# Performance work log

Measured on AMD Instinct MI355X. Metric: run time of the kernel, lower is better.

Reference implementation:

```python
import jax, jax.numpy as jnp
import numpy as np

DIM = 96
HEADS = 3
HEAD_DIM = 32
MLP_DIM = 384
WS = 4  # window size (cubic)


def _rel_indices(ws):
    # relative position indices for a ws^3 window, offset to [0, 2*ws-2]
    coords = np.stack(np.meshgrid(np.arange(ws), np.arange(ws), np.arange(ws), indexing='ij'), -1).reshape(-1, 3)
    rel = coords[:, None, :] - coords[None, :, :] + (ws - 1)  # (n, n, 3)
    return jnp.asarray(rel, dtype=jnp.int32)


def _layer_norm(x, g, b, eps=1e-5):
    m = x.mean(-1, keepdims=True)
    v = x.var(-1, keepdims=True)
    return (x - m) * jax.lax.rsqrt(v + eps) * g + b


def setup_inputs() -> dict:
    key = jax.random.key(0)
    ks = jax.random.split(key, 12)
    inner = HEADS * HEAD_DIM
    s = lambda fan_in: 1.0 / np.sqrt(fan_in)
    return {
        'x': jax.random.normal(ks[0], (2, 128, 128, 8, DIM), dtype=jnp.float32),
        'ln1_g': jnp.ones((DIM,), jnp.float32),
        'ln1_b': jnp.zeros((DIM,), jnp.float32),
        'w_qkv': jax.random.normal(ks[1], (DIM, 3 * inner), jnp.float32) * s(DIM),
        'w_out': jax.random.normal(ks[2], (inner, DIM), jnp.float32) * s(inner),
        'b_out': jnp.zeros((DIM,), jnp.float32),
        'pos_tab': jax.random.normal(ks[3], (2 * WS - 1, 2 * WS - 1, 2 * WS - 1), jnp.float32),
        'ln2_g': jnp.ones((DIM,), jnp.float32),
        'ln2_b': jnp.zeros((DIM,), jnp.float32),
        'w1': jax.random.normal(ks[4], (DIM, MLP_DIM), jnp.float32) * s(DIM),
        'b1': jnp.zeros((MLP_DIM,), jnp.float32),
        'w2': jax.random.normal(ks[5], (MLP_DIM, DIM), jnp.float32) * s(MLP_DIM),
        'b2': jnp.zeros((DIM,), jnp.float32),
    }


def reference(x, ln1_g, ln1_b, w_qkv, w_out, b_out, pos_tab, ln2_g, ln2_b, w1, b1, w2, b2):
    B, H, W, D, C = x.shape
    h, d, ws = HEADS, HEAD_DIM, WS
    nH, nW, nD = H // ws, W // ws, D // ws
    n = ws ** 3
    scale = d ** -0.5

    # --- window attention block (PreNorm + Residual) ---
    y = _layer_norm(x, ln1_g, ln1_b)
    qkv = y @ w_qkv  # (B,H,W,D,3*h*d)
    qkv = qkv.reshape(B, nH, ws, nW, ws, nD, ws, 3, h, d)
    qkv = qkv.transpose(7, 0, 8, 1, 3, 5, 2, 4, 6, 9)  # (3,B,h,nH,nW,nD,ws,ws,ws,d)
    qkv = qkv.reshape(3, B, h, nH * nW * nD, n, d)
    q, k, v = qkv[0], qkv[1], qkv[2]

    attn = jnp.einsum('bhwid,bhwjd->bhwij', q, k) * scale  # (B,h,nw,n,n)
    rel = _rel_indices(ws)
    bias = pos_tab[rel[..., 0], rel[..., 1], rel[..., 2]]  # (n,n)
    attn = jax.nn.softmax(attn + bias, axis=-1)
    o = jnp.einsum('bhwij,bhwjd->bhwid', attn, v)  # (B,h,nw,n,d)

    o = o.reshape(B, h, nH, nW, nD, ws, ws, ws, d)
    o = o.transpose(0, 2, 5, 3, 6, 4, 7, 1, 8).reshape(B, H, W, D, h * d)
    x = x + (o @ w_out + b_out)

    # --- MLP block (PreNorm + Residual), GELU exact to match nn.GELU ---
    y = _layer_norm(x, ln2_g, ln2_b)
    y = jax.nn.gelu(y @ w1 + b1, approximate=False) @ w2 + b2
    return x + y
```

## Files before the change

### kernel.cpp

```cpp
#include <hip/hip_runtime.h>

#define DIM 96
#define HEADS 3
#define HD 32
#define MLPD 384
#define NTOK 64
#define YP 104
#define KP 104
#define QKP 200
#define VP 72
#define WSP 104
#define HP 40
#define W1P 104
#define W2P 40
#define W2SP 32
#define X1P 100
#define CH 32
#define NCH 12
#define WQT_OFF 147456
#define WOT_OFF 175104
#define WS2_NEEDED 368640

typedef unsigned short ushort_t;
typedef unsigned int uint_t;
typedef __attribute__((ext_vector_type(8))) short bf16x8;
typedef __attribute__((ext_vector_type(4))) float f32x4;

__device__ inline float b2f(ushort_t u) {
    return __uint_as_float(((uint_t)u) << 16);
}
__device__ inline ushort_t f2b(float f) {
    uint_t u = __float_as_uint(f);
    uint_t r = u + 0x7FFFu + ((u >> 16) & 1u);
    return (ushort_t)(r >> 16);
}
__device__ inline void split2(float v, ushort_t& hi, ushort_t& lo) {
    hi = f2b(v);
    float d = v - b2f(hi);
    lo = f2b(d);
}
__device__ inline void split_pack2(float v0, float v1, uint_t& hi2, uint_t& lo2) {
    uint_t u0 = __float_as_uint(v0), u1 = __float_as_uint(v1);
    hi2 = __builtin_amdgcn_perm(u1, u0, 0x07060302u);
    float d0 = v0 - __uint_as_float(u0 & 0xFFFF0000u);
    float d1 = v1 - __uint_as_float(u1 & 0xFFFF0000u);
    lo2 = __builtin_amdgcn_perm(__float_as_uint(d1), __float_as_uint(d0), 0x07060302u);
}
__device__ inline size_t grow(int bb, int wh, int ww, int wd, int t) {
    return ((size_t)((bb * 128 + wh * 4 + (t >> 4)) * 128 + ww * 4 + ((t >> 2) & 3)) * 8
            + wd * 4 + (t & 3));
}
__device__ inline float gelu_fast(float v) {
    float z = v * 0.70710678118654752f;
    float az = fabsf(z);
    float k = __frcp_rn(1.0f + 0.3275911f * az);
    float poly = k * (0.254829592f + k * (-0.284496736f + k * (1.421413741f
                 + k * (-1.453152027f + k * 1.061405429f))));
    float e = 1.0f - poly * __expf(-az * az);
    float erfv = copysignf(e, z);
    return 0.5f * v * (1.0f + erfv);
}

__global__ __launch_bounds__(256) void prep_weights(
    const float* __restrict__ w1, const float* __restrict__ w2,
    const float* __restrict__ w_qkv, const float* __restrict__ w_out,
    ushort_t* __restrict__ wt)
{
    int idx = blockIdx.x * 256 + threadIdx.x;
    if (idx >= 96 * MLPD) return;
    {
        int k = idx / MLPD, col = idx % MLPD;
        ushort_t h, l;
        split2(w1[idx], h, l);
        wt[col * 96 + k] = h;
        wt[36864 + col * 96 + k] = l;
    }
    {
        int k = idx / 96, n = idx % 96;
        int c = k >> 5, f = k & 31;
        int p = ((f & 15) >> 2) * 8 + (f >> 4) * 4 + (f & 3);
        ushort_t h, l;
        split2(w2[idx], h, l);
        wt[73728  + n * MLPD + c * 32 + p] = h;
        wt[110592 + n * MLPD + c * 32 + p] = l;
    }
    if (idx < 288 * 96) {
        int f = idx / 96, k = idx % 96;
        wt[WQT_OFF + f * 96 + k] = f2b(w_qkv[k * 288 + f]);
    }
    if (idx < 96 * 96) {
        int n = idx / 96, k = idx % 96;
        wt[WOT_OFF + n * 96 + k] = f2b(w_out[k * 96 + n]);
    }
}

__global__ __launch_bounds__(256, 4) void swin_fused_kernel(
    const float* __restrict__ x,
    const float* __restrict__ ln1_g, const float* __restrict__ ln1_b,
    const ushort_t* __restrict__ wt,
    const float* __restrict__ b_out, const float* __restrict__ pos_tab,
    const float* __restrict__ ln2_g, const float* __restrict__ ln2_b,
    const float* __restrict__ b1v, const float* __restrict__ b2v,
    float* __restrict__ out)
{
    __shared__ __align__(16) ushort_t smem[20224];
    ushort_t* ybuf = smem;
    ushort_t* kbuf = smem + 6656;
    ushort_t* vbuf = smem + 13312;
    float* x1f = reinterpret_cast<float*>(smem + 6656);

    const ushort_t* wqkvt = wt + WQT_OFF;
    const ushort_t* woutt = wt + WOT_OFF;

    const int tid = threadIdx.x;
    const int wv = tid >> 6;
    const int lane = tid & 63;
    const int lr = lane & 15;
    const int lk = lane >> 4;

    const int wid = blockIdx.x;
    const int wd = wid & 1;
    const int ww = (wid >> 1) & 31;
    const int wh = (wid >> 6) & 31;
    const int bb = wid >> 11;

    float breg[4][4];
    {
        const int cb = lr >> 2, cc = lr & 3;
        #pragma unroll
        for (int nt = 0; nt < 4; ++nt)
            #pragma unroll
            for (int r = 0; r < 4; ++r)
                breg[nt][r] = pos_tab[((wv - nt + 3) * 7 + (lk - cb + 3)) * 7 + (r - cc + 3)];
    }

    {
        const int t = tid >> 2, part = tid & 3;
        const float* xr = x + grow(bb, wh, ww, wd, t) * DIM + part * 24;
        float vals[24];
        #pragma unroll
        for (int i = 0; i < 6; ++i) {
            float4 v4 = *reinterpret_cast<const float4*>(xr + i * 4);
            vals[i * 4 + 0] = v4.x; vals[i * 4 + 1] = v4.y;
            vals[i * 4 + 2] = v4.z; vals[i * 4 + 3] = v4.w;
        }
        float s = 0.f, sq = 0.f;
        #pragma unroll
        for (int i = 0; i < 24; ++i) { s += vals[i]; sq += vals[i] * vals[i]; }
        s  += __shfl_xor(s, 1);  s  += __shfl_xor(s, 2);
        sq += __shfl_xor(sq, 1); sq += __shfl_xor(sq, 2);
        float mean = s * (1.f / 96.f);
        float var  = sq * (1.f / 96.f) - mean * mean;
        float rstd = rsqrtf(var + 1e-5f);
        #pragma unroll
        for (int i = 0; i < 24; i += 2) {
            int c = part * 24 + i;
            float v0 = (vals[i]     - mean) * rstd * ln1_g[c]     + ln1_b[c];
            float v1 = (vals[i + 1] - mean) * rstd * ln1_g[c + 1] + ln1_b[c + 1];
            *reinterpret_cast<uint_t*>(&ybuf[t * YP + c]) =
                (uint_t)f2b(v0) | ((uint_t)f2b(v1) << 16);
        }
    }
    asm volatile("s_waitcnt lgkmcnt(0)" ::: "memory");

    bf16x8 ay[3];
    #pragma unroll
    for (int ks = 0; ks < 3; ++ks)
        ay[ks] = *reinterpret_cast<const bf16x8*>(&ybuf[(wv * 16 + lr) * YP + ks * 32 + lk * 8]);

    #pragma unroll 3
    for (int ch = 0; ch < 9; ++ch) {
        #pragma unroll
        for (int nt = 0; nt < 2; ++nt) {
            const int feat = ch * 32 + nt * 16 + lr;
            const ushort_t* wb = &wqkvt[feat * 96 + lk * 8];
            bf16x8 b0 = *reinterpret_cast<const bf16x8*>(wb);
            bf16x8 b1 = *reinterpret_cast<const bf16x8*>(wb + 32);
            bf16x8 b2 = *reinterpret_cast<const bf16x8*>(wb + 64);
            f32x4 acc = (f32x4){0.f, 0.f, 0.f, 0.f};
            acc = __builtin_amdgcn_mfma_f32_16x16x32_bf16(ay[0], b0, acc, 0, 0, 0);
            acc = __builtin_amdgcn_mfma_f32_16x16x32_bf16(ay[1], b1, acc, 0, 0, 0);
            acc = __builtin_amdgcn_mfma_f32_16x16x32_bf16(ay[2], b2, acc, 0, 0, 0);
            if (ch < 3) {
                #pragma unroll
                for (int r = 0; r < 4; ++r)
                    ybuf[(wv * 16 + lk * 4 + r) * YP + feat] = f2b(acc[r]);
            } else if (ch < 6) {
                #pragma unroll
                for (int r = 0; r < 4; ++r)
                    kbuf[(wv * 16 + lk * 4 + r) * KP + (feat - 96)] = f2b(acc[r]);
            } else {
                #pragma unroll
                for (int r = 0; r < 4; ++r)
                    vbuf[(feat - 192) * VP + wv * 16 + lk * 4 + r] = f2b(acc[r]);
            }
        }
    }
    __syncthreads();

    bf16x8 aq[3];
    #pragma unroll
    for (int h = 0; h < HEADS; ++h)
        aq[h] = *reinterpret_cast<const bf16x8*>(&ybuf[(wv * 16 + lr) * YP + h * HD + lk * 8]);
    asm volatile("s_waitcnt lgkmcnt(0)" ::: "memory");

    const float scale = 0.17677669529663687f;
    f32x4 oacc[6];
    #pragma unroll
    for (int i = 0; i < 6; ++i) oacc[i] = (f32x4){0.f, 0.f, 0.f, 0.f};
    ushort_t* pb = &ybuf[wv * 16 * YP];

    #pragma unroll
    for (int h = 0; h < HEADS; ++h) {
        float s[4][4];
        #pragma unroll
        for (int nt = 0; nt < 4; ++nt) {
            bf16x8 bk = *reinterpret_cast<const bf16x8*>(&kbuf[(nt * 16 + lr) * KP + h * HD + lk * 8]);
            f32x4 acc = (f32x4){0.f, 0.f, 0.f, 0.f};
            acc = __builtin_amdgcn_mfma_f32_16x16x32_bf16(aq[h], bk, acc, 0, 0, 0);
            #pragma unroll
            for (int r = 0; r < 4; ++r) s[nt][r] = acc[r] * scale + breg[nt][r];
        }
        float m[4], sum[4], inv[4];
        #pragma unroll
        for (int r = 0; r < 4; ++r) {
            m[r] = fmaxf(fmaxf(s[0][r], s[1][r]), fmaxf(s[2][r], s[3][r]));
            for (int mk = 1; mk < 16; mk <<= 1) m[r] = fmaxf(m[r], __shfl_xor(m[r], mk));
        }
        #pragma unroll
        for (int r = 0; r < 4; ++r) sum[r] = 0.f;
        #pragma unroll
        for (int nt = 0; nt < 4; ++nt)
            #pragma unroll
            for (int r = 0; r < 4; ++r) { s[nt][r] = __expf(s[nt][r] - m[r]); sum[r] += s[nt][r]; }
        #pragma unroll
        for (int r = 0; r < 4; ++r) {
            for (int mk = 1; mk < 16; mk <<= 1) sum[r] += __shfl_xor(sum[r], mk);
            inv[r] = 1.f / sum[r];
        }
        #pragma unroll
        for (int nt = 0; nt < 4; ++nt)
            #pragma unroll
            for (int r = 0; r < 4; ++r)
                pb[(lk * 4 + r) * VP + nt * 16 + lr] = f2b(s[nt][r] * inv[r]);
        asm volatile("s_waitcnt lgkmcnt(0)" ::: "memory");

        bf16x8 pa0 = *reinterpret_cast<const bf16x8*>(&pb[lr * VP + 0 * 32 + lk * 8]);
        bf16x8 pa1 = *reinterpret_cast<const bf16x8*>(&pb[lr * VP + 1 * 32 + lk * 8]);
        #pragma unroll
        for (int nt2 = 0; nt2 < 2; ++nt2) {
            f32x4 acc = oacc[h * 2 + nt2];
            bf16x8 bv0 = *reinterpret_cast<const bf16x8*>(&vbuf[(h * HD + nt2 * 16 + lr) * VP + 0 * 32 + lk * 8]);
            bf16x8 bv1 = *reinterpret_cast<const bf16x8*>(&vbuf[(h * HD + nt2 * 16 + lr) * VP + 1 * 32 + lk * 8]);
            acc = __builtin_amdgcn_mfma_f32_16x16x32_bf16(pa0, bv0, acc, 0, 0, 0);
            acc = __builtin_amdgcn_mfma_f32_16x16x32_bf16(pa1, bv1, acc, 0, 0, 0);
            oacc[h * 2 + nt2] = acc;
        }
    }
    __syncthreads();

    const ushort_t* g1[3]; ushort_t* l1[3];
    const ushort_t* g2[3]; ushort_t* l2[3];
    #pragma unroll
    for (int i = 0; i < 3; ++i) {
        int o = tid + i * 256;
        int p = o / 384, rem = o % 384;
        {
            int rr = rem / 12, j = rem % 12;
            g1[i] = wt + p * 36864 + rr * 96 + j * 8;
            l1[i] = &ybuf[p * 3328 + rr * 104 + j * 8];
        }
        {
            int n = rem / 4, j = rem % 4;
            int jsw = j ^ ((n >> 1) & 3);
            g2[i] = wt + 73728 + p * 36864 + n * 384 + j * 8;
            l2[i] = &ybuf[p * 3072 + n * W2SP + jsw * 8];
        }
    }
    bf16x8 pf1[3], pf2[3];
    #pragma unroll
    for (int i = 0; i < 3; ++i) pf1[i] = *reinterpret_cast<const bf16x8*>(g1[i]);
    #pragma unroll
    for (int i = 0; i < 3; ++i) pf2[i] = *reinterpret_cast<const bf16x8*>(g2[i]);

    #pragma unroll
    for (int nt = 0; nt < 6; ++nt)
        #pragma unroll
        for (int r = 0; r < 4; ++r)
            ybuf[(wv * 16 + lk * 4 + r) * YP + nt * 16 + lr] = f2b(oacc[nt][r]);
    asm volatile("s_waitcnt lgkmcnt(0)" ::: "memory");

    bf16x8 ao[3];
    #pragma unroll
    for (int ks = 0; ks < 3; ++ks)
        ao[ks] = *reinterpret_cast<const bf16x8*>(&ybuf[(wv * 16 + lr) * YP + ks * 32 + lk * 8]);
    #pragma unroll
    for (int nt = 0; nt < 6; ++nt) {
        const ushort_t* wb = &woutt[(nt * 16 + lr) * 96 + lk * 8];
        f32x4 acc = (f32x4){0.f, 0.f, 0.f, 0.f};
        acc = __builtin_amdgcn_mfma_f32_16x16x32_bf16(ao[0], *reinterpret_cast<const bf16x8*>(wb), acc, 0, 0, 0);
        acc = __builtin_amdgcn_mfma_f32_16x16x32_bf16(ao[1], *reinterpret_cast<const bf16x8*>(wb + 32), acc, 0, 0, 0);
        acc = __builtin_amdgcn_mfma_f32_16x16x32_bf16(ao[2], *reinterpret_cast<const bf16x8*>(wb + 64), acc, 0, 0, 0);
        int col = nt * 16 + lr;
        float bias = b_out[col];
        #pragma unroll
        for (int r = 0; r < 4; ++r) {
            int t = wv * 16 + lk * 4 + r;
            x1f[t * X1P + col] = acc[r] + bias + x[grow(bb, wh, ww, wd, t) * DIM + col];
        }
    }
    asm volatile("s_waitcnt lgkmcnt(0)" ::: "memory");

    bf16x8 ah[3], al[3];
    {
        const int row = wv * 16 + lr;
        float v[3][8];
        float s = 0.f, sq = 0.f;
        #pragma unroll
        for (int ks = 0; ks < 3; ++ks) {
            float4 a4 = *reinterpret_cast<const float4*>(&x1f[row * X1P + ks * 32 + lk * 8]);
            float4 b4 = *reinterpret_cast<const float4*>(&x1f[row * X1P + ks * 32 + lk * 8 + 4]);
            v[ks][0] = a4.x; v[ks][1] = a4.y; v[ks][2] = a4.z; v[ks][3] = a4.w;
            v[ks][4] = b4.x; v[ks][5] = b4.y; v[ks][6] = b4.z; v[ks][7] = b4.w;
            #pragma unroll
            for (int j = 0; j < 8; ++j) { s += v[ks][j]; sq += v[ks][j] * v[ks][j]; }
        }
        s  += __shfl_xor(s, 16);  s  += __shfl_xor(s, 32);
        sq += __shfl_xor(sq, 16); sq += __shfl_xor(sq, 32);
        float mean = s * (1.f / 96.f);
        float var  = sq * (1.f / 96.f) - mean * mean;
        float rstd = rsqrtf(var + 1e-5f);
        #pragma unroll
        for (int ks = 0; ks < 3; ++ks) {
            float4 g4a = *reinterpret_cast<const float4*>(&ln2_g[ks * 32 + lk * 8]);
            float4 g4b = *reinterpret_cast<const float4*>(&ln2_g[ks * 32 + lk * 8 + 4]);
            float4 b4a = *reinterpret_cast<const float4*>(&ln2_b[ks * 32 + lk * 8]);
            float4 b4b = *reinterpret_cast<const float4*>(&ln2_b[ks * 32 + lk * 8 + 4]);
            float g[8] = {g4a.x, g4a.y, g4a.z, g4a.w, g4b.x, g4b.y, g4b.z, g4b.w};
            float bbv[8] = {b4a.x, b4a.y, b4a.z, b4a.w, b4b.x, b4b.y, b4b.z, b4b.w};
            float y[8];
            #pragma unroll
            for (int j = 0; j < 8; ++j)
                y[j] = (v[ks][j] - mean) * rstd * g[j] + bbv[j];
            union { uint4 u; bf16x8 f; } H, L;
            split_pack2(y[0], y[1], H.u.x, L.u.x);
            split_pack2(y[2], y[3], H.u.y, L.u.y);
            split_pack2(y[4], y[5], H.u.z, L.u.z);
            split_pack2(y[6], y[7], H.u.w, L.u.w);
            ah[ks] = H.f;
            al[ks] = L.f;
        }
    }

    f32x4 macc[6];
    #pragma unroll
    for (int nt = 0; nt < 6; ++nt) macc[nt] = (f32x4){0.f, 0.f, 0.f, 0.f};

    for (int c = 0; c < NCH; ++c) {
        __syncthreads();
        #pragma unroll
        for (int i = 0; i < 3; ++i)
            *reinterpret_cast<bf16x8*>(l1[i]) = pf1[i];
        if (c + 1 < NCH) {
            const int coff1 = (c + 1) * 3072;
            #pragma unroll
            for (int i = 0; i < 3; ++i)
                pf1[i] = *reinterpret_cast<const bf16x8*>(g1[i] + coff1);
        }
        __syncthreads();

        f32x4 hpre[2];
        #pragma unroll
        for (int nt = 0; nt < 2; ++nt) {
            const int roff = (nt * 16 + lr) * 104 + lk * 8;
            bf16x8 wh0 = *reinterpret_cast<const bf16x8*>(&ybuf[roff]);
            bf16x8 wh1 = *reinterpret_cast<const bf16x8*>(&ybuf[roff + 32]);
            bf16x8 wh2 = *reinterpret_cast<const bf16x8*>(&ybuf[roff + 64]);
            bf16x8 wl0 = *reinterpret_cast<const bf16x8*>(&ybuf[3328 + roff]);
            bf16x8 wl1 = *reinterpret_cast<const bf16x8*>(&ybuf[3328 + roff + 32]);
            bf16x8 wl2 = *reinterpret_cast<const bf16x8*>(&ybuf[3328 + roff + 64]);
            f32x4 acc = (f32x4){0.f, 0.f, 0.f, 0.f};
            acc = __builtin_amdgcn_mfma_f32_16x16x32_bf16(wh0, ah[0], acc, 0, 0, 0);
            acc = __builtin_amdgcn_mfma_f32_16x16x32_bf16(wh0, al[0], acc, 0, 0, 0);
            acc = __builtin_amdgcn_mfma_f32_16x16x32_bf16(wl0, ah[0], acc, 0, 0, 0);
            acc = __builtin_amdgcn_mfma_f32_16x16x32_bf16(wh1, ah[1], acc, 0, 0, 0);
            acc = __builtin_amdgcn_mfma_f32_16x16x32_bf16(wh1, al[1], acc, 0, 0, 0);
            acc = __builtin_amdgcn_mfma_f32_16x16x32_bf16(wl1, ah[1], acc, 0, 0, 0);
            acc = __builtin_amdgcn_mfma_f32_16x16x32_bf16(wh2, ah[2], acc, 0, 0, 0);
            acc = __builtin_amdgcn_mfma_f32_16x16x32_bf16(wh2, al[2], acc, 0, 0, 0);
            acc = __builtin_amdgcn_mfma_f32_16x16x32_bf16(wl2, ah[2], acc, 0, 0, 0);
            hpre[nt] = acc;
        }

        float4 b40 = *reinterpret_cast<const float4*>(&b1v[c * CH + 0 * 16 + lk * 4]);
        float4 b41 = *reinterpret_cast<const float4*>(&b1v[c * CH + 1 * 16 + lk * 4]);
        bf16x8 a2h, a2l;
        {
            float g0 = gelu_fast(hpre[0][0] + b40.x);
            float g1v = gelu_fast(hpre[0][1] + b40.y);
            float g2v = gelu_fast(hpre[0][2] + b40.z);
            float g3 = gelu_fast(hpre[0][3] + b40.w);
            float g4 = gelu_fast(hpre[1][0] + b41.x);
            float g5 = gelu_fast(hpre[1][1] + b41.y);
            float g6 = gelu_fast(hpre[1][2] + b41.z);
            float g7 = gelu_fast(hpre[1][3] + b41.w);
            union { uint4 u; bf16x8 f; } H, L;
            split_pack2(g0, g1v, H.u.x, L.u.x);
            split_pack2(g2v, g3, H.u.y, L.u.y);
            split_pack2(g4, g5, H.u.z, L.u.z);
            split_pack2(g6, g7, H.u.w, L.u.w);
            a2h = H.f;
            a2l = L.f;
        }

        __syncthreads();
        #pragma unroll
        for (int i = 0; i < 3; ++i)
            *reinterpret_cast<bf16x8*>(l2[i]) = pf2[i];
        if (c + 1 < NCH) {
            const int coff2 = (c + 1) * 32;
            #pragma unroll
            for (int i = 0; i < 3; ++i)
                pf2[i] = *reinterpret_cast<const bf16x8*>(g2[i] + coff2);
        }
        __syncthreads();

        #pragma unroll
        for (int nt2 = 0; nt2 < 6; ++nt2) {
            const int row2 = nt2 * 16 + lr;
            const int sw2 = (lk ^ ((row2 >> 1) & 3)) * 8;
            bf16x8 wh2v = *reinterpret_cast<const bf16x8*>(&ybuf[row2 * W2SP + sw2]);
            bf16x8 wl2v = *reinterpret_cast<const bf16x8*>(&ybuf[3072 + row2 * W2SP + sw2]);
            f32x4 acc = macc[nt2];
            acc = __builtin_amdgcn_mfma_f32_16x16x32_bf16(a2h, wh2v, acc, 0, 0, 0);
            acc = __builtin_amdgcn_mfma_f32_16x16x32_bf16(a2h, wl2v, acc, 0, 0, 0);
            acc = __builtin_amdgcn_mfma_f32_16x16x32_bf16(a2l, wh2v, acc, 0, 0, 0);
            macc[nt2] = acc;
        }
    }

    #pragma unroll
    for (int nt = 0; nt < 6; ++nt) {
        int col = nt * 16 + lr;
        float bias = b2v[col];
        #pragma unroll
        for (int r = 0; r < 4; ++r) {
            int t = wv * 16 + lk * 4 + r;
            out[grow(bb, wh, ww, wd, t) * DIM + col] =
                macc[nt][r] + bias + x1f[t * X1P + col];
        }
    }
}

__global__ __launch_bounds__(256) void attn_mfma_kernel(
    const float* __restrict__ x,
    const float* __restrict__ ln1_g, const float* __restrict__ ln1_b,
    const float* __restrict__ w_qkv,
    const float* __restrict__ w_out, const float* __restrict__ b_out,
    const float* __restrict__ pos_tab,
    float* __restrict__ out)
{
    __shared__ ushort_t ybuf[NTOK * YP];
    __shared__ ushort_t qkbuf[NTOK * QKP];
    __shared__ ushort_t vbuf[96 * VP];
    __shared__ ushort_t wstage[CH * WSP];
    __shared__ float pos[343];

    const int tid = threadIdx.x;
    const int wv = tid >> 6;
    const int lane = tid & 63;
    const int lr = lane & 15;
    const int lk = lane >> 4;

    const int wid = blockIdx.x;
    const int wd = wid & 1;
    const int ww = (wid >> 1) & 31;
    const int wh = (wid >> 6) & 31;
    const int bb = wid >> 11;

    for (int e = tid; e < 343; e += 256) pos[e] = pos_tab[e];

    {
        const int t = tid >> 2, part = tid & 3;
        const float* xr = x + grow(bb, wh, ww, wd, t) * DIM + part * 24;
        float vals[24];
        for (int i = 0; i < 6; ++i) {
            float4 v4 = *reinterpret_cast<const float4*>(xr + i * 4);
            vals[i * 4 + 0] = v4.x; vals[i * 4 + 1] = v4.y;
            vals[i * 4 + 2] = v4.z; vals[i * 4 + 3] = v4.w;
        }
        float s = 0.f, sq = 0.f;
        for (int i = 0; i < 24; ++i) { s += vals[i]; sq += vals[i] * vals[i]; }
        s  += __shfl_xor(s, 1);  s  += __shfl_xor(s, 2);
        sq += __shfl_xor(sq, 1); sq += __shfl_xor(sq, 2);
        float mean = s * (1.f / 96.f);
        float var  = sq * (1.f / 96.f) - mean * mean;
        float rstd = rsqrtf(var + 1e-5f);
        for (int i = 0; i < 24; i += 2) {
            int c = part * 24 + i;
            float v0 = (vals[i]     - mean) * rstd * ln1_g[c]     + ln1_b[c];
            float v1 = (vals[i + 1] - mean) * rstd * ln1_g[c + 1] + ln1_b[c + 1];
            *reinterpret_cast<uint_t*>(&ybuf[t * YP + c]) =
                (uint_t)f2b(v0) | ((uint_t)f2b(v1) << 16);
        }
    }
    __syncthreads();

    bf16x8 ay[3];
    for (int ks = 0; ks < 3; ++ks)
        ay[ks] = *reinterpret_cast<const bf16x8*>(&ybuf[(wv * 16 + lr) * YP + ks * 32 + lk * 8]);

    for (int ch = 0; ch < 9; ++ch) {
        for (int e = tid; e < 32 * 48; e += 256) {
            int n = e & 31, kp = e >> 5;
            float a = w_qkv[(2 * kp) * 288 + ch * 32 + n];
            float b = w_qkv[(2 * kp + 1) * 288 + ch * 32 + n];
            *reinterpret_cast<uint_t*>(&wstage[n * WSP + 2 * kp]) =
                (uint_t)f2b(a) | ((uint_t)f2b(b) << 16);
        }
        __syncthreads();

        for (int nt = 0; nt < 2; ++nt) {
            f32x4 acc = (f32x4){0.f, 0.f, 0.f, 0.f};
            for (int ks = 0; ks < 3; ++ks) {
                bf16x8 bf = *reinterpret_cast<const bf16x8*>(&wstage[(nt * 16 + lr) * WSP + ks * 32 + lk * 8]);
                acc = __builtin_amdgcn_mfma_f32_16x16x32_bf16(ay[ks], bf, acc, 0, 0, 0);
            }
            int feat = ch * 32 + nt * 16 + lr;
            if (ch < 6) {
                for (int r = 0; r < 4; ++r)
                    qkbuf[(wv * 16 + lk * 4 + r) * QKP + feat] = f2b(acc[r]);
            } else {
                for (int r = 0; r < 4; ++r)
                    vbuf[(feat - 192) * VP + wv * 16 + lk * 4 + r] = f2b(acc[r]);
            }
        }
        __syncthreads();
    }

    float breg[4][4];
    {
        const int cb = lr >> 2, cc = lr & 3;
        for (int nt = 0; nt < 4; ++nt)
            for (int r = 0; r < 4; ++r)
                breg[nt][r] = pos[((wv - nt + 3) * 7 + (lk - cb + 3)) * 7 + (r - cc + 3)];
    }

    const float scale = 0.17677669529663687f;
    f32x4 oacc[6];
    for (int i = 0; i < 6; ++i) oacc[i] = (f32x4){0.f, 0.f, 0.f, 0.f};
    ushort_t* pb = &ybuf[wv * 16 * VP];

    for (int h = 0; h < HEADS; ++h) {
        bf16x8 aq = *reinterpret_cast<const bf16x8*>(&qkbuf[(wv * 16 + lr) * QKP + h * HD + lk * 8]);
        float s[4][4];
        for (int nt = 0; nt < 4; ++nt) {
            bf16x8 bk = *reinterpret_cast<const bf16x8*>(&qkbuf[(nt * 16 + lr) * QKP + 96 + h * HD + lk * 8]);
            f32x4 acc = (f32x4){0.f, 0.f, 0.f, 0.f};
            acc = __builtin_amdgcn_mfma_f32_16x16x32_bf16(aq, bk, acc, 0, 0, 0);
            for (int r = 0; r < 4; ++r) s[nt][r] = acc[r] * scale + breg[nt][r];
        }
        float m[4], sum[4], inv[4];
        for (int r = 0; r < 4; ++r) {
            m[r] = fmaxf(fmaxf(s[0][r], s[1][r]), fmaxf(s[2][r], s[3][r]));
            for (int mk = 1; mk < 16; mk <<= 1) m[r] = fmaxf(m[r], __shfl_xor(m[r], mk));
        }
        for (int r = 0; r < 4; ++r) sum[r] = 0.f;
        for (int nt = 0; nt < 4; ++nt)
            for (int r = 0; r < 4; ++r) { s[nt][r] = __expf(s[nt][r] - m[r]); sum[r] += s[nt][r]; }
        for (int r = 0; r < 4; ++r) {
            for (int mk = 1; mk < 16; mk <<= 1) sum[r] += __shfl_xor(sum[r], mk);
            inv[r] = 1.f / sum[r];
        }
        for (int nt = 0; nt < 4; ++nt)
            for (int r = 0; r < 4; ++r)
                pb[(lk * 4 + r) * VP + nt * 16 + lr] = f2b(s[nt][r] * inv[r]);
        asm volatile("s_waitcnt lgkmcnt(0)" ::: "memory");

        bf16x8 pa0 = *reinterpret_cast<const bf16x8*>(&pb[lr * VP + 0 * 32 + lk * 8]);
        bf16x8 pa1 = *reinterpret_cast<const bf16x8*>(&pb[lr * VP + 1 * 32 + lk * 8]);
        for (int nt2 = 0; nt2 < 2; ++nt2) {
            f32x4 acc = oacc[h * 2 + nt2];
            bf16x8 bv0 = *reinterpret_cast<const bf16x8*>(&vbuf[(h * HD + nt2 * 16 + lr) * VP + 0 * 32 + lk * 8]);
            bf16x8 bv1 = *reinterpret_cast<const bf16x8*>(&vbuf[(h * HD + nt2 * 16 + lr) * VP + 1 * 32 + lk * 8]);
            acc = __builtin_amdgcn_mfma_f32_16x16x32_bf16(pa0, bv0, acc, 0, 0, 0);
            acc = __builtin_amdgcn_mfma_f32_16x16x32_bf16(pa1, bv1, acc, 0, 0, 0);
            oacc[h * 2 + nt2] = acc;
        }
    }
    __syncthreads();

    for (int nt = 0; nt < 6; ++nt)
        for (int r = 0; r < 4; ++r)
            ybuf[(wv * 16 + lk * 4 + r) * YP + nt * 16 + lr] = f2b(oacc[nt][r]);
    for (int e = tid; e < 96 * 48; e += 256) {
        int n = e % 96, kp = e / 96;
        float a = w_out[(2 * kp) * 96 + n];
        float b = w_out[(2 * kp + 1) * 96 + n];
        *reinterpret_cast<uint_t*>(&qkbuf[n * WSP + 2 * kp]) =
            (uint_t)f2b(a) | ((uint_t)f2b(b) << 16);
    }
    __syncthreads();

    bf16x8 ao[3];
    for (int ks = 0; ks < 3; ++ks)
        ao[ks] = *reinterpret_cast<const bf16x8*>(&ybuf[(wv * 16 + lr) * YP + ks * 32 + lk * 8]);
    for (int nt = 0; nt < 6; ++nt) {
        f32x4 acc = (f32x4){0.f, 0.f, 0.f, 0.f};
        for (int ks = 0; ks < 3; ++ks) {
            bf16x8 bw = *reinterpret_cast<const bf16x8*>(&qkbuf[(nt * 16 + lr) * WSP + ks * 32 + lk * 8]);
            acc = __builtin_amdgcn_mfma_f32_16x16x32_bf16(ao[ks], bw, acc, 0, 0, 0);
        }
        int col = nt * 16 + lr;
        float bias = b_out[col];
        for (int r = 0; r < 4; ++r) {
            int t = wv * 16 + lk * 4 + r;
            size_t g = grow(bb, wh, ww, wd, t);
            out[g * DIM + col] = acc[r] + bias + x[g * DIM + col];
        }
    }
}

__global__ __launch_bounds__(256) void mlp_stage_kernel(
    float* __restrict__ io,
    const float* __restrict__ ln2_g, const float* __restrict__ ln2_b,
    const float* __restrict__ w1, const float* __restrict__ b1v,
    const float* __restrict__ w2, const float* __restrict__ b2v)
{
    __shared__ ushort_t yhi[NTOK * YP], ylo[NTOK * YP];
    __shared__ ushort_t hhi[NTOK * HP], hlo[NTOK * HP];
    __shared__ ushort_t whi[96 * HP],  wlo[96 * HP];

    const int tid = threadIdx.x;
    const int wv = tid >> 6;
    const int lane = tid & 63;
    const int lr = lane & 15;
    const int lk = lane >> 4;
    const size_t base = (size_t)blockIdx.x * NTOK * DIM;

    {
        const int t = tid >> 2, part = tid & 3;
        const float* xr = io + base + t * DIM + part * 24;
        float vals[24];
        for (int i = 0; i < 6; ++i) {
            float4 v4 = *reinterpret_cast<const float4*>(xr + i * 4);
            vals[i * 4 + 0] = v4.x; vals[i * 4 + 1] = v4.y;
            vals[i * 4 + 2] = v4.z; vals[i * 4 + 3] = v4.w;
        }
        float s = 0.f, sq = 0.f;
        for (int i = 0; i < 24; ++i) { s += vals[i]; sq += vals[i] * vals[i]; }
        s  += __shfl_xor(s, 1);  s  += __shfl_xor(s, 2);
        sq += __shfl_xor(sq, 1); sq += __shfl_xor(sq, 2);
        float mean = s * (1.f / 96.f);
        float var  = sq * (1.f / 96.f) - mean * mean;
        float rstd = rsqrtf(var + 1e-5f);
        for (int i = 0; i < 24; i += 2) {
            int c = part * 24 + i;
            float v0 = (vals[i]     - mean) * rstd * ln2_g[c]     + ln2_b[c];
            float v1 = (vals[i + 1] - mean) * rstd * ln2_g[c + 1] + ln2_b[c + 1];
            ushort_t h0, l0, h1, l1;
            split2(v0, h0, l0); split2(v1, h1, l1);
            *reinterpret_cast<uint_t*>(&yhi[t * YP + c]) = (uint_t)h0 | ((uint_t)h1 << 16);
            *reinterpret_cast<uint_t*>(&ylo[t * YP + c]) = (uint_t)l0 | ((uint_t)l1 << 16);
        }
    }

    f32x4 oacc[6];
    for (int nt = 0; nt < 6; ++nt) oacc[nt] = (f32x4){0.f, 0.f, 0.f, 0.f};

    for (int c = 0; c < NCH; ++c) {
        for (int idx = tid; idx < CH * 96; idx += 256) {
            int col = idx & 31, k = idx >> 5;
            ushort_t h, l;
            split2(w1[k * MLPD + c * CH + col], h, l);
            whi[col * W1P + k] = h;
            wlo[col * W1P + k] = l;
        }
        __syncthreads();

        bf16x8 ah[3], al[3];
        for (int ks = 0; ks < 3; ++ks) {
            ah[ks] = *reinterpret_cast<const bf16x8*>(&yhi[(wv * 16 + lr) * YP + ks * 32 + lk * 8]);
            al[ks] = *reinterpret_cast<const bf16x8*>(&ylo[(wv * 16 + lr) * YP + ks * 32 + lk * 8]);
        }
        for (int nt = 0; nt < 2; ++nt) {
            f32x4 acc = (f32x4){0.f, 0.f, 0.f, 0.f};
            for (int ks = 0; ks < 3; ++ks) {
                bf16x8 bh = *reinterpret_cast<const bf16x8*>(&whi[(nt * 16 + lr) * W1P + ks * 32 + lk * 8]);
                bf16x8 bl = *reinterpret_cast<const bf16x8*>(&wlo[(nt * 16 + lr) * W1P + ks * 32 + lk * 8]);
                acc = __builtin_amdgcn_mfma_f32_16x16x32_bf16(ah[ks], bh, acc, 0, 0, 0);
                acc = __builtin_amdgcn_mfma_f32_16x16x32_bf16(ah[ks], bl, acc, 0, 0, 0);
                acc = __builtin_amdgcn_mfma_f32_16x16x32_bf16(al[ks], bh, acc, 0, 0, 0);
            }
            float bias = b1v[c * CH + nt * 16 + lr];
            for (int r = 0; r < 4; ++r) {
                float ge = gelu_fast(acc[r] + bias);
                ushort_t h, l;
                split2(ge, h, l);
                hhi[(wv * 16 + lk * 4 + r) * HP + nt * 16 + lr] = h;
                hlo[(wv * 16 + lk * 4 + r) * HP + nt * 16 + lr] = l;
            }
        }
        __syncthreads();

        for (int idx = tid; idx < 96 * CH; idx += 256) {
            int n = idx % 96, k = idx / 96;
            ushort_t h, l;
            split2(w2[(c * CH + k) * DIM + n], h, l);
            whi[n * W2P + k] = h;
            wlo[n * W2P + k] = l;
        }
        __syncthreads();

        bf16x8 a2h = *reinterpret_cast<const bf16x8*>(&hhi[(wv * 16 + lr) * HP + lk * 8]);
        bf16x8 a2l = *reinterpret_cast<const bf16x8*>(&hlo[(wv * 16 + lr) * HP + lk * 8]);
        for (int nt = 0; nt < 6; ++nt) {
            f32x4 acc = oacc[nt];
            bf16x8 bh = *reinterpret_cast<const bf16x8*>(&whi[(nt * 16 + lr) * W2P + lk * 8]);
            bf16x8 bl = *reinterpret_cast<const bf16x8*>(&wlo[(nt * 16 + lr) * W2P + lk * 8]);
            acc = __builtin_amdgcn_mfma_f32_16x16x32_bf16(a2h, bh, acc, 0, 0, 0);
            acc = __builtin_amdgcn_mfma_f32_16x16x32_bf16(a2h, bl, acc, 0, 0, 0);
            acc = __builtin_amdgcn_mfma_f32_16x16x32_bf16(a2l, bh, acc, 0, 0, 0);
            oacc[nt] = acc;
        }
        __syncthreads();
    }

    for (int nt = 0; nt < 6; ++nt) {
        float bias = b2v[nt * 16 + lr];
        for (int r = 0; r < 4; ++r) {
            size_t gi = base + (size_t)(wv * 16 + lk * 4 + r) * DIM + nt * 16 + lr;
            io[gi] = oacc[nt][r] + bias + io[gi];
        }
    }
}

extern "C" void kernel_launch(void* const* d_in, const int* in_sizes, int n_in,
                              void* d_out, int out_size, void* d_ws, size_t ws_size,
                              hipStream_t stream) {
    const float* x      = (const float*)d_in[0];
    const float* ln1_g  = (const float*)d_in[1];
    const float* ln1_b  = (const float*)d_in[2];
    const float* w_qkv  = (const float*)d_in[3];
    const float* w_out  = (const float*)d_in[4];
    const float* b_out  = (const float*)d_in[5];
    const float* pos    = (const float*)d_in[6];
    const float* ln2_g  = (const float*)d_in[7];
    const float* ln2_b  = (const float*)d_in[8];
    const float* w1     = (const float*)d_in[9];
    const float* b1v    = (const float*)d_in[10];
    const float* w2     = (const float*)d_in[11];
    const float* b2v    = (const float*)d_in[12];
    float* out = (float*)d_out;

    if (ws_size >= (size_t)WS2_NEEDED) {
        ushort_t* wt = (ushort_t*)d_ws;
        prep_weights<<<(96 * MLPD + 255) / 256, 256, 0, stream>>>(w1, w2, w_qkv, w_out, wt);
        swin_fused_kernel<<<4096, 256, 0, stream>>>(
            x, ln1_g, ln1_b, wt, b_out, pos, ln2_g, ln2_b, b1v, b2v, out);
    } else {
        attn_mfma_kernel<<<4096, 256, 0, stream>>>(
            x, ln1_g, ln1_b, w_qkv, w_out, b_out, pos, out);
        mlp_stage_kernel<<<4096, 256, 0, stream>>>(out, ln2_g, ln2_b, w1, b1v, w2, b2v);
    }
}
```

Measured before the change: 268.2 us.

## Stage W2 chunk in separate LDS region to drop per-chunk barrier pair

Moves the W2 weight staging buffer from the shared ybuf region into the region that previously held x1 (kbuf area), so W1 and W2 chunks can be written to LDS in the same phase. This removes one pair of __syncthreads per MLP chunk iteration. To free that region, the residual x1 values are kept in registers (x1r) for the final output add instead of being reread from LDS. It increases register pressure under the 4-waves launch bound and may risk spills.

```diff
diff --git a/kernel.cpp b/kernel.cpp
--- a/kernel.cpp
+++ b/kernel.cpp
@@ -108,6 +108,7 @@
     ushort_t* kbuf = smem + 6656;
     ushort_t* vbuf = smem + 13312;
     float* x1f = reinterpret_cast<float*>(smem + 6656);
+    ushort_t* w2s = smem + 6656;
 
     const ushort_t* wqkvt = wt + WQT_OFF;
     const ushort_t* woutt = wt + WOT_OFF;
@@ -274,7 +275,7 @@
             int n = rem / 4, j = rem % 4;
             int jsw = j ^ ((n >> 1) & 3);
             g2[i] = wt + 73728 + p * 36864 + n * 384 + j * 8;
-            l2[i] = &ybuf[p * 3072 + n * W2SP + jsw * 8];
+            l2[i] = &w2s[p * 3072 + n * W2SP + jsw * 8];
         }
     }
     bf16x8 pf1[3], pf2[3];
@@ -294,6 +295,8 @@
     #pragma unroll
     for (int ks = 0; ks < 3; ++ks)
         ao[ks] = *reinterpret_cast<const bf16x8*>(&ybuf[(wv * 16 + lr) * YP + ks * 32 + lk * 8]);
+
+    f32x4 x1r[6];
     #pragma unroll
     for (int nt = 0; nt < 6; ++nt) {
         const ushort_t* wb = &woutt[(nt * 16 + lr) * 96 + lk * 8];
@@ -306,7 +309,9 @@
         #pragma unroll
         for (int r = 0; r < 4; ++r) {
             int t = wv * 16 + lk * 4 + r;
-            x1f[t * X1P + col] = acc[r] + bias + x[grow(bb, wh, ww, wd, t) * DIM + col];
+            float v = acc[r] + bias + x[grow(bb, wh, ww, wd, t) * DIM + col];
+            x1r[nt][r] = v;
+            x1f[t * X1P + col] = v;
         }
     }
     asm volatile("s_waitcnt lgkmcnt(0)" ::: "memory");
@@ -351,6 +356,7 @@
             al[ks] = L.f;
         }
     }
+    asm volatile("s_waitcnt lgkmcnt(0)" ::: "memory");
 
     f32x4 macc[6];
     #pragma unroll
@@ -359,13 +365,17 @@
     for (int c = 0; c < NCH; ++c) {
         __syncthreads();
         #pragma unroll
-        for (int i = 0; i < 3; ++i)
+        for (int i = 0; i < 3; ++i) {
             *reinterpret_cast<bf16x8*>(l1[i]) = pf1[i];
+            *reinterpret_cast<bf16x8*>(l2[i]) = pf2[i];
+        }
         if (c + 1 < NCH) {
-            const int coff1 = (c + 1) * 3072;
+            const int coff1 = (c + 1) * 3072, coff2 = (c + 1) * 32;
             #pragma unroll
-            for (int i = 0; i < 3; ++i)
+            for (int i = 0; i < 3; ++i) {
                 pf1[i] = *reinterpret_cast<const bf16x8*>(g1[i] + coff1);
+                pf2[i] = *reinterpret_cast<const bf16x8*>(g2[i] + coff2);
+            }
         }
         __syncthreads();
 
@@ -413,24 +423,12 @@
             a2l = L.f;
         }
 
-        __syncthreads();
-        #pragma unroll
-        for (int i = 0; i < 3; ++i)
-            *reinterpret_cast<bf16x8*>(l2[i]) = pf2[i];
-        if (c + 1 < NCH) {
-            const int coff2 = (c + 1) * 32;
-            #pragma unroll
-            for (int i = 0; i < 3; ++i)
-                pf2[i] = *reinterpret_cast<const bf16x8*>(g2[i] + coff2);
-        }
-        __syncthreads();
-
         #pragma unroll
         for (int nt2 = 0; nt2 < 6; ++nt2) {
             const int row2 = nt2 * 16 + lr;
             const int sw2 = (lk ^ ((row2 >> 1) & 3)) * 8;
-            bf16x8 wh2v = *reinterpret_cast<const bf16x8*>(&ybuf[row2 * W2SP + sw2]);
-            bf16x8 wl2v = *reinterpret_cast<const bf16x8*>(&ybuf[3072 + row2 * W2SP + sw2]);
+            bf16x8 wh2v = *reinterpret_cast<const bf16x8*>(&w2s[row2 * W2SP + sw2]);
+            bf16x8 wl2v = *reinterpret_cast<const bf16x8*>(&w2s[3072 + row2 * W2SP + sw2]);
             f32x4 acc = macc[nt2];
             acc = __builtin_amdgcn_mfma_f32_16x16x32_bf16(a2h, wh2v, acc, 0, 0, 0);
             acc = __builtin_amdgcn_mfma_f32_16x16x32_bf16(a2h, wl2v, acc, 0, 0, 0);
@@ -447,7 +445,7 @@
         for (int r = 0; r < 4; ++r) {
             int t = wv * 16 + lk * 4 + r;
             out[grow(bb, wh, ww, wd, t) * DIM + col] =
-                macc[nt][r] + bias + x1f[t * X1P + col];
+                macc[nt][r] + bias + x1r[nt][r];
         }
     }
 }
```

Measured after the change: 301.5 us. 1.12x slower.
